# Performance work log

Hardware: AMD Instinct MI355X
Metric: run time of the kernel (lower is better)

## Reference

```python
import jax, jax.numpy as jnp
import numpy as np

B, L, C, K, S = 8, 4096, 512, 5, 8


def setup_inputs() -> dict:
    key = jax.random.key(0)
    ks = jax.random.split(key, 5)
    x = jax.random.normal(ks[0], (B, L, C), dtype=jnp.float32)
    # contiguous random partition of [0, L) into S segments per batch row
    rng = np.random.default_rng(0)
    cuts = np.sort(rng.integers(1, L, size=(B, S - 1)), axis=1)
    starts = np.concatenate([np.zeros((B, 1), np.int64), cuts.astype(np.int64)], axis=1)
    ends = np.concatenate([cuts.astype(np.int64), np.full((B, 1), L, np.int64)], axis=1)
    segment_boundaries = jnp.asarray(np.stack([starts, ends], axis=-1))  # [B,S,2]
    fan = 1.0 / np.sqrt(K)
    w_dw = jax.random.normal(ks[1], (C, K), dtype=jnp.float32) * fan
    b_dw = jax.random.normal(ks[2], (C,), dtype=jnp.float32) * 0.01
    w_pw = jax.random.normal(ks[3], (C, C), dtype=jnp.float32) * (1.0 / np.sqrt(C))
    b_pw = jax.random.normal(ks[4], (C,), dtype=jnp.float32) * 0.01
    return {"x": x, "segment_boundaries": segment_boundaries,
            "w_dw": w_dw, "b_dw": b_dw, "w_pw": w_pw, "b_pw": b_pw}


def reference(x, segment_boundaries, w_dw, b_dw, w_pw, b_pw):
    # x: [B,L,C]; segment_boundaries: [B,S,2]; w_dw: [C,K]; w_pw: [C_out,C_in]
    Bx, Lx, Cx = x.shape
    Kx = w_dw.shape[1]
    starts = segment_boundaries[..., 0]  # [B,S]
    ends = segment_boundaries[..., 1]    # [B,S]
    pos = jnp.arange(Lx)
    in_seg = (pos[None, None, :] >= starts[..., None]) & (pos[None, None, :] < ends[..., None])  # [B,S,L]
    covered = in_seg.any(axis=1)                                  # [B,L]
    seg_id = jnp.where(covered, jnp.argmax(in_seg, axis=1), -1)   # [B,L]

    # causal depthwise conv with left zero-pad per segment (no cross-segment leakage)
    acc = jnp.zeros_like(x)
    for d in range(Kx):  # d = how far back we look; tap index = K-1-d
        if d == 0:
            x_s, id_s = x, seg_id
        else:
            x_s = jnp.pad(x, ((0, 0), (d, 0), (0, 0)))[:, :Lx]
            id_s = jnp.pad(seg_id, ((0, 0), (d, 0)), constant_values=-2)[:, :Lx]
        m = ((seg_id == id_s) & covered).astype(x.dtype)          # [B,L]
        acc = acc + w_dw[:, Kx - 1 - d] * x_s * m[..., None]
    dw = acc + b_dw                                               # [B,L,C]
    pw = jnp.einsum('blc,dc->bld', dw, w_pw) + b_pw               # pointwise 1x1 conv
    return pw * covered[..., None].astype(x.dtype)                # zeros outside segments
```

## Files before the change

kernel.cpp:

```cpp
#include <hip/hip_runtime.h>
#include <hip/hip_bf16.h>

typedef __bf16 bf16;
typedef __bf16 bf16x2 __attribute__((ext_vector_type(2)));
typedef __bf16 bf16x4 __attribute__((ext_vector_type(4)));
typedef __bf16 bf16x8 __attribute__((ext_vector_type(8)));
typedef float f32x4 __attribute__((ext_vector_type(4)));

#define NB 8
#define L_ 4096
#define C_ 512
#define KW 5
#define NS 8
#define BM 128
#define BN 512
#define BK 32
#define NT 1024
#define KSTEPS 16

#define GLOAD_LDS16(g, l)                                                      \
  __builtin_amdgcn_global_load_lds(                                            \
      (const __attribute__((address_space(1))) void*)(g),                      \
      (__attribute__((address_space(3))) void*)(l), 16, 0, 0)

#define PRE_BARRIER(N)                                                         \
  do {                                                                         \
    asm volatile("s_waitcnt vmcnt(" #N ") lgkmcnt(0)" ::: "memory");           \
    __builtin_amdgcn_sched_barrier(0);                                         \
    __builtin_amdgcn_s_barrier();                                              \
    __builtin_amdgcn_sched_barrier(0);                                         \
  } while (0)

__global__ __launch_bounds__(256) void prep_kernel(
    const float* __restrict__ w_pw, const float* __restrict__ b_dw,
    const float* __restrict__ b_pw, bf16* __restrict__ wbf,
    float* __restrict__ bias2) {
  const int n = blockIdx.x;
  const int t = threadIdx.x;
  float2 v = *(const float2*)(w_pw + n * C_ + 2 * t);
  bf16x2 hv;
  hv[0] = (bf16)v.x;
  hv[1] = (bf16)v.y;
  *(bf16x2*)(wbf + n * C_ + 2 * t) = hv;
  float2 bb = *(const float2*)(b_dw + 2 * t);
  float s = v.x * bb.x + v.y * bb.y;
#pragma unroll
  for (int off = 32; off; off >>= 1) s += __shfl_down(s, off, 64);
  __shared__ float part[4];
  if ((t & 63) == 0) part[t >> 6] = s;
  __syncthreads();
  if (t == 0) bias2[n] = b_pw[n] + part[0] + part[1] + part[2] + part[3];
}

__global__ __launch_bounds__(NT) void fused_dwconv_gemm(
    const float* __restrict__ x, const int* __restrict__ segb,
    const float* __restrict__ w_dw, const bf16* __restrict__ wbf,
    const float* __restrict__ bias2, float* __restrict__ out) {
  __shared__ __align__(16) bf16 Bs[2][BN * BK];
  __shared__ __align__(16) bf16 dws[2][BM][40];
  __shared__ __align__(16) float xs[2][BM + 4][BK];
  __shared__ __align__(16) float wdt[KW][C_];
  __shared__ int segst[BM];

  const int t = threadIdx.x;
  const int lane = t & 63;
  const int wid = t >> 6;
  const int wm = wid >> 2;
  const int wn = wid & 3;

  const int b = blockIdx.x >> 5;
  const int l0 = (blockIdx.x & 31) << 7;

  if (t < C_) {
#pragma unroll
    for (int d = 0; d < KW; ++d) wdt[d][t] = w_dw[t * KW + d];
  }
  if (t < BM) {
    int l = l0 + t;
    const int* sb = segb + b * NS * 2;
    int st = 0;
#pragma unroll
    for (int s = 0; s < NS; ++s) {
      int a0 = sb[2 * s], a1 = sb[2 * s + 1];
      if (l >= a0 && l < a1) st = a0;
    }
    segst[t] = st;
  }
  __syncthreads();

  const int gr = t >> 3;
  const int gc = t & 7;
  int nv = (l0 + gr) - segst[gr];
  if (nv > 4) nv = 4;
  const bool fast = __all(nv == 4);

  const float* gxp = x + (size_t)(b * L_ + l0 + gr) * C_ + gc * 4;
  const int h = wid * 2 + lane;
  const int hr = h >> 3, hc = h & 7;
  int hl = l0 - 4 + hr;
  if (hl < 0) hl = 0;
  const float* gxh = x + (size_t)(b * L_ + hl) * C_ + hc * 4;

  const int nB0 = t >> 2, cB0 = t & 3;
  const int nB1 = (NT + t) >> 2, cB1 = t & 3;
  const bf16* gB0 = wbf + (size_t)nB0 * C_ + (cB0 ^ ((nB0 >> 1) & 3)) * 8;
  const bf16* gB1 = wbf + (size_t)nB1 * C_ + (cB1 ^ ((nB1 >> 1) & 3)) * 8;
  const int dB0 = (t & ~63) * 8;
  const int dB1 = (NT + (t & ~63)) * 8;

  f32x4 acc[2][8];
#pragma unroll
  for (int i = 0; i < 2; ++i)
#pragma unroll
    for (int j = 0; j < 8; ++j) acc[i][j] = (f32x4){0.f, 0.f, 0.f, 0.f};

  auto issueB = [&](int kk) {
    bf16* base = (bf16*)Bs[kk & 1];
    GLOAD_LDS16(gB0 + kk * BK, base + dB0);
    GLOAD_LDS16(gB1 + kk * BK, base + dB1);
  };

  auto issueGX = [&](int kk, float4& m4, float4& h4) {
    m4 = *(const float4*)(gxp + kk * BK);
    if (lane < 2) h4 = *(const float4*)(gxh + kk * BK);
  };

  auto stageX = [&](int kk, const float4& m4, const float4& h4) {
    const int p = kk & 1;
    *(float4*)&xs[p][gr + 4][gc * 4] = m4;
    if (lane < 2) *(float4*)&xs[p][hr][hc * 4] = h4;
  };

  auto conv = [&](int kk) {
    const int p = kk & 1;
    const int k0c = kk * BK + gc * 4;
    float w[KW][4];
#pragma unroll
    for (int m = 0; m < KW; ++m) {
      float4 wv = *(const float4*)&wdt[m][k0c];
      w[m][0] = wv.x; w[m][1] = wv.y; w[m][2] = wv.z; w[m][3] = wv.w;
    }
    if (!fast) {
#pragma unroll
      for (int m = 0; m < KW; ++m)
#pragma unroll
        for (int i = 0; i < 4; ++i)
          w[m][i] = (4 - m <= nv) ? w[m][i] : 0.f;
    }
    f32x4 a = (f32x4){0.f, 0.f, 0.f, 0.f};
#pragma unroll
    for (int m = 0; m < KW; ++m) {
      f32x4 xv = *(const f32x4*)&xs[p][gr + m][gc * 4];
#pragma unroll
      for (int i = 0; i < 4; ++i) a[i] = fmaf(w[m][i], xv[i], a[i]);
    }
    bf16x4 hq;
#pragma unroll
    for (int i = 0; i < 4; ++i) hq[i] = (bf16)a[i];
    *(bf16x4*)&dws[p][gr][gc * 4] = hq;
  };

  auto mma = [&](int kk) {
    const int p = kk & 1;
    bf16x8 afr[2];
#pragma unroll
    for (int mf = 0; mf < 2; ++mf)
      afr[mf] = *(const bf16x8*)&dws[p][wm * 32 + mf * 16 + (lane & 15)]
                                     [(lane >> 4) * 8];
#pragma unroll
    for (int nf = 0; nf < 8; ++nf) {
      const int nl = wn * 128 + nf * 16 + (lane & 15);
      const int ph = (lane >> 4) ^ ((nl >> 1) & 3);
      bf16x8 bfr = *(const bf16x8*)&Bs[p][nl * 32 + ph * 8];
#pragma unroll
      for (int mf = 0; mf < 2; ++mf)
        acc[mf][nf] = __builtin_amdgcn_mfma_f32_16x16x32_bf16(
            afr[mf], bfr, acc[mf][nf], 0, 0, 0);
    }
  };

  float4 gm0, gm1, gh0, gh1;

  issueGX(0, gm0, gh0);
  issueGX(1, gm1, gh1);
  stageX(0, gm0, gh0);
  issueGX(2, gm0, gh0);
  PRE_BARRIER(4);
  stageX(1, gm1, gh1);
  issueB(0);
  issueGX(3, gm1, gh1);
  conv(0);
  PRE_BARRIER(2);

#pragma unroll 1
  for (int k2 = 0; k2 < 12; k2 += 2) {
    issueB(k2 + 1);
    stageX(k2 + 2, gm0, gh0);
    issueGX(k2 + 4, gm0, gh0);
    conv(k2 + 1);
    mma(k2);
    PRE_BARRIER(2);

    issueB(k2 + 2);
    stageX(k2 + 3, gm1, gh1);
    issueGX(k2 + 5, gm1, gh1);
    conv(k2 + 2);
    mma(k2 + 1);
    PRE_BARRIER(2);
  }
  issueB(13);
  stageX(14, gm0, gh0);
  conv(13);
  mma(12);
  PRE_BARRIER(0);
  issueB(14);
  stageX(15, gm1, gh1);
  conv(14);
  mma(13);
  PRE_BARRIER(0);
  issueB(15);
  conv(15);
  mma(14);
  PRE_BARRIER(0);
  mma(15);

  const int col0 = wn * 128 + (lane & 15);
  float bia[8];
#pragma unroll
  for (int nf = 0; nf < 8; ++nf) bia[nf] = bias2[col0 + nf * 16];
  const int rb0 = l0 + wm * 32 + ((lane >> 4) << 2);
#pragma unroll
  for (int mf = 0; mf < 2; ++mf) {
#pragma unroll
    for (int i = 0; i < 4; ++i) {
      const int row = rb0 + mf * 16 + i;
      float* o = out + (size_t)(b * L_ + row) * C_ + col0;
#pragma unroll
      for (int nf = 0; nf < 8; ++nf) o[nf * 16] = acc[mf][nf][i] + bia[nf];
    }
  }
}

extern "C" void kernel_launch(void* const* d_in, const int* in_sizes, int n_in,
                              void* d_out, int out_size, void* d_ws,
                              size_t ws_size, hipStream_t stream) {
  const float* x = (const float*)d_in[0];
  const int* segb = (const int*)d_in[1];
  const float* w_dw = (const float*)d_in[2];
  const float* b_dw = (const float*)d_in[3];
  const float* w_pw = (const float*)d_in[4];
  const float* b_pw = (const float*)d_in[5];
  float* out = (float*)d_out;

  bf16* wbf = (bf16*)d_ws;
  float* bias2 = (float*)((char*)d_ws + C_ * C_ * 2);

  prep_kernel<<<C_, 256, 0, stream>>>(w_pw, b_dw, b_pw, wbf, bias2);
  fused_dwconv_gemm<<<NB * L_ / BM, NT, 0, stream>>>(x, segb, w_dw, wbf,
                                                     bias2, out);
}
```

Baseline: 46.59 us.

## Split fused depthwise conv and GEMM into separate conv and GEMM kernels

Adds a standalone conv kernel that computes the causal segmented depthwise conv with a sliding register window and writes a bf16 intermediate to workspace. A separate GEMM kernel then streams that intermediate and the bf16 weights into a triple-buffered LDS pipeline using direct global-to-LDS loads, with a different warp tiling. The aim is to take conv work and fp32 x staging out of the GEMM critical loop. The cost is an extra 32 MB bf16 round trip through global memory and one more launch. The old fused kernel remains as a fallback when the workspace is too small.

```diff
diff --git a/kernel.cpp b/kernel.cpp
--- a/kernel.cpp
+++ b/kernel.cpp
@@ -1,5 +1,6 @@
 #include <hip/hip_runtime.h>
 #include <hip/hip_bf16.h>
+#include <climits>
 
 typedef __bf16 bf16;
 typedef __bf16 bf16x2 __attribute__((ext_vector_type(2)));
@@ -12,16 +13,15 @@
 #define C_ 512
 #define KW 5
 #define NS 8
-#define BM 128
-#define BN 512
-#define BK 32
-#define NT 1024
-#define KSTEPS 16
 
 #define GLOAD_LDS16(g, l)                                                      \
   __builtin_amdgcn_global_load_lds(                                            \
       (const __attribute__((address_space(1))) void*)(g),                      \
       (__attribute__((address_space(3))) void*)(l), 16, 0, 0)
+#define GLOAD_LDS4(g, l)                                                       \
+  __builtin_amdgcn_global_load_lds(                                            \
+      (const __attribute__((address_space(1))) void*)(g),                      \
+      (__attribute__((address_space(3))) void*)(l), 4, 0, 0)
 
 #define PRE_BARRIER(N)                                                         \
   do {                                                                         \
@@ -52,6 +52,207 @@
   if (t == 0) bias2[n] = b_pw[n] + part[0] + part[1] + part[2] + part[3];
 }
 
+__global__ __launch_bounds__(256) void conv_kernel(
+    const float* __restrict__ x, const int* __restrict__ segb,
+    const float* __restrict__ w_dw, bf16* __restrict__ dwg) {
+  const int g = blockIdx.x * 256 + threadIdx.x;
+  const int quad = g & 127;
+  const int rest = g >> 7;
+  const int b = rest >> 7;
+  const int chunk = rest & 127;
+  const int l0 = chunk << 5;
+
+  float4 raw[5];
+#pragma unroll
+  for (int i = 0; i < 5; ++i)
+    raw[i] = *(const float4*)(w_dw + quad * 20 + i * 4);
+  f32x4 wt[5];
+#pragma unroll
+  for (int m = 0; m < 5; ++m)
+#pragma unroll
+    for (int i = 0; i < 4; ++i) {
+      const int f = i * 5 + m;
+      wt[m][i] = ((const float*)&raw[f >> 2])[f & 3];
+    }
+
+  const int* sb = segb + b * NS * 2;
+  int stv[NS];
+#pragma unroll
+  for (int s = 0; s < NS; ++s) stv[s] = sb[2 * s];
+  auto nxt = [&](int l) {
+    int nn = INT_MAX;
+#pragma unroll
+    for (int s = 0; s < NS; ++s)
+      nn = (stv[s] > l && stv[s] < nn) ? stv[s] : nn;
+    return nn;
+  };
+  int ns = nxt(l0 - 4);
+
+  const float* xbase = x + ((size_t)(b * L_ + l0)) * C_ + quad * 4;
+  bf16* dbase = dwg + ((size_t)(b * L_ + l0)) * C_ + quad * 4;
+
+  const f32x4 z4 = (f32x4){0.f, 0.f, 0.f, 0.f};
+  f32x4 w0 = z4, w1 = z4, w2 = z4, w3 = z4;
+
+#pragma unroll
+  for (int i = 0; i < 4; ++i) {
+    const int l = l0 - 4 + i;
+    f32x4 nv = z4;
+    if (l >= 0) nv = *(const f32x4*)(xbase + (ptrdiff_t)(i - 4) * C_);
+    if (l == ns) { w0 = z4; w1 = z4; w2 = z4; w3 = z4; ns = nxt(l); }
+    w0 = w1; w1 = w2; w2 = w3; w3 = nv;
+  }
+
+  auto dorow = [&](int l, f32x4& A, f32x4& B4, f32x4& Cc, f32x4& D,
+                   const f32x4& E, int off) {
+    if (l == ns) { A = z4; B4 = z4; Cc = z4; D = z4; ns = nxt(l); }
+    f32x4 r;
+#pragma unroll
+    for (int i = 0; i < 4; ++i) {
+      float a = A[i] * wt[0][i];
+      a = fmaf(B4[i], wt[1][i], a);
+      a = fmaf(Cc[i], wt[2][i], a);
+      a = fmaf(D[i], wt[3][i], a);
+      a = fmaf(E[i], wt[4][i], a);
+      r[i] = a;
+    }
+    bf16x4 h;
+#pragma unroll
+    for (int i = 0; i < 4; ++i) h[i] = (bf16)r[i];
+    *(bf16x4*)(dbase + (size_t)off * C_) = h;
+  };
+
+#pragma unroll 1
+  for (int g8 = 0; g8 < 8; ++g8) {
+    const int lb = l0 + g8 * 4;
+    f32x4 n0 = *(const f32x4*)(xbase + (ptrdiff_t)(g8 * 4 + 0) * C_);
+    f32x4 n1 = *(const f32x4*)(xbase + (ptrdiff_t)(g8 * 4 + 1) * C_);
+    f32x4 n2 = *(const f32x4*)(xbase + (ptrdiff_t)(g8 * 4 + 2) * C_);
+    f32x4 n3 = *(const f32x4*)(xbase + (ptrdiff_t)(g8 * 4 + 3) * C_);
+    dorow(lb + 0, w0, w1, w2, w3, n0, g8 * 4 + 0);
+    dorow(lb + 1, w1, w2, w3, n0, n1, g8 * 4 + 1);
+    dorow(lb + 2, w2, w3, n0, n1, n2, g8 * 4 + 2);
+    dorow(lb + 3, w3, n0, n1, n2, n3, g8 * 4 + 3);
+    w0 = n0; w1 = n1; w2 = n2; w3 = n3;
+  }
+}
+
+#define BMg 128
+#define BNg 512
+#define BKg 32
+__global__ __launch_bounds__(1024) void gemm_kernel(
+    const bf16* __restrict__ dwg, const bf16* __restrict__ wbf,
+    const float* __restrict__ bias2, float* __restrict__ out) {
+  __shared__ __align__(16) bf16 As[3][BMg * BKg];
+  __shared__ __align__(16) bf16 Bs[3][BNg * BKg];
+
+  const int t = threadIdx.x;
+  const int lane = t & 63;
+  const int wid = t >> 6;
+  const int wm = wid >> 3;
+  const int wn = wid & 7;
+
+  const int b = blockIdx.x >> 5;
+  const int l0 = (blockIdx.x & 31) << 7;
+
+  const int rA0 = t >> 4, wAi = t & 15;
+  const int rA1 = 64 + (t >> 4);
+  const size_t aoff0 = (size_t)(b * L_ + l0 + rA0) * C_ +
+                       ((((wAi >> 2) ^ ((rA0 >> 1) & 3)) << 3) + ((wAi & 3) << 1));
+  const size_t aoff1 = (size_t)(b * L_ + l0 + rA1) * C_ +
+                       ((((wAi >> 2) ^ ((rA1 >> 1) & 3)) << 3) + ((wAi & 3) << 1));
+  const int dA0 = wid * 128;
+  const int dA1 = 2048 + wid * 128;
+
+  const int nB0 = t >> 2, cB0 = t & 3;
+  const int nB1 = 256 + (t >> 2);
+  const bf16* gB0 = wbf + (size_t)nB0 * C_ + (cB0 ^ ((nB0 >> 1) & 3)) * 8;
+  const bf16* gB1 = wbf + (size_t)nB1 * C_ + (cB0 ^ ((nB1 >> 1) & 3)) * 8;
+  const int dB0 = (t & ~63) * 8;
+  const int dB1 = (1024 + (t & ~63)) * 8;
+
+  int aOff[4], bOff[4];
+#pragma unroll
+  for (int mf = 0; mf < 4; ++mf) {
+    const int row = wm * 64 + mf * 16 + (lane & 15);
+    aOff[mf] = row * 32 + (((lane >> 4) ^ ((row >> 1) & 3)) << 3);
+  }
+#pragma unroll
+  for (int nf = 0; nf < 4; ++nf) {
+    const int nl = wn * 64 + nf * 16 + (lane & 15);
+    bOff[nf] = nl * 32 + (((lane >> 4) ^ ((nl >> 1) & 3)) << 3);
+  }
+
+  f32x4 acc[4][4];
+#pragma unroll
+  for (int i = 0; i < 4; ++i)
+#pragma unroll
+    for (int j = 0; j < 4; ++j) acc[i][j] = (f32x4){0.f, 0.f, 0.f, 0.f};
+
+  auto issueAB = [&](int kk, int p) {
+    const int k0 = kk * BKg;
+    bf16* a = (bf16*)As[p];
+    bf16* bb = (bf16*)Bs[p];
+    GLOAD_LDS4(dwg + aoff0 + k0, a + dA0);
+    GLOAD_LDS4(dwg + aoff1 + k0, a + dA1);
+    GLOAD_LDS16(gB0 + k0, bb + dB0);
+    GLOAD_LDS16(gB1 + k0, bb + dB1);
+  };
+
+  auto mma = [&](int p) {
+    const bf16* a = (const bf16*)As[p];
+    const bf16* bb = (const bf16*)Bs[p];
+    bf16x8 afr[4];
+#pragma unroll
+    for (int mf = 0; mf < 4; ++mf) afr[mf] = *(const bf16x8*)(a + aOff[mf]);
+    __builtin_amdgcn_s_setprio(1);
+#pragma unroll
+    for (int nf = 0; nf < 4; ++nf) {
+      bf16x8 bfr = *(const bf16x8*)(bb + bOff[nf]);
+#pragma unroll
+      for (int mf = 0; mf < 4; ++mf)
+        acc[mf][nf] = __builtin_amdgcn_mfma_f32_16x16x32_bf16(
+            afr[mf], bfr, acc[mf][nf], 0, 0, 0);
+    }
+    __builtin_amdgcn_s_setprio(0);
+  };
+
+  issueAB(0, 0);
+  int pc = 0, pn = 1;
+#pragma unroll 1
+  for (int k = 0; k < 16; ++k) {
+    if (k < 15) {
+      issueAB(k + 1, pn);
+      PRE_BARRIER(4);
+    } else {
+      PRE_BARRIER(0);
+    }
+    mma(pc);
+    pc = (pc == 2) ? 0 : pc + 1;
+    pn = (pn == 2) ? 0 : pn + 1;
+  }
+
+  const int col0 = wn * 64 + (lane & 15);
+  float bia[4];
+#pragma unroll
+  for (int nf = 0; nf < 4; ++nf) bia[nf] = bias2[col0 + nf * 16];
+  const int rb0 = l0 + wm * 64 + ((lane >> 4) << 2);
+#pragma unroll
+  for (int mf = 0; mf < 4; ++mf) {
+#pragma unroll
+    for (int i = 0; i < 4; ++i) {
+      const int row = rb0 + mf * 16 + i;
+      float* o = out + (size_t)(b * L_ + row) * C_ + col0;
+#pragma unroll
+      for (int nf = 0; nf < 4; ++nf) o[nf * 16] = acc[mf][nf][i] + bia[nf];
+    }
+  }
+}
+
+#define BM 128
+#define BN 512
+#define BK 32
+#define NT 1024
 __global__ __launch_bounds__(NT) void fused_dwconv_gemm(
     const float* __restrict__ x, const int* __restrict__ segb,
     const float* __restrict__ w_dw, const bf16* __restrict__ wbf,
@@ -67,7 +268,6 @@
   const int wid = t >> 6;
   const int wm = wid >> 2;
   const int wn = wid & 3;
-
   const int b = blockIdx.x >> 5;
   const int l0 = (blockIdx.x & 31) << 7;
 
@@ -102,9 +302,9 @@
   const float* gxh = x + (size_t)(b * L_ + hl) * C_ + hc * 4;
 
   const int nB0 = t >> 2, cB0 = t & 3;
-  const int nB1 = (NT + t) >> 2, cB1 = t & 3;
+  const int nB1 = (NT + t) >> 2;
   const bf16* gB0 = wbf + (size_t)nB0 * C_ + (cB0 ^ ((nB0 >> 1) & 3)) * 8;
-  const bf16* gB1 = wbf + (size_t)nB1 * C_ + (cB1 ^ ((nB1 >> 1) & 3)) * 8;
+  const bf16* gB1 = wbf + (size_t)nB1 * C_ + (cB0 ^ ((nB1 >> 1) & 3)) * 8;
   const int dB0 = (t & ~63) * 8;
   const int dB1 = (NT + (t & ~63)) * 8;
 
@@ -119,18 +319,15 @@
     GLOAD_LDS16(gB0 + kk * BK, base + dB0);
     GLOAD_LDS16(gB1 + kk * BK, base + dB1);
   };
-
   auto issueGX = [&](int kk, float4& m4, float4& h4) {
     m4 = *(const float4*)(gxp + kk * BK);
     if (lane < 2) h4 = *(const float4*)(gxh + kk * BK);
   };
-
   auto stageX = [&](int kk, const float4& m4, const float4& h4) {
     const int p = kk & 1;
     *(float4*)&xs[p][gr + 4][gc * 4] = m4;
     if (lane < 2) *(float4*)&xs[p][hr][hc * 4] = h4;
   };
-
   auto conv = [&](int kk) {
     const int p = kk & 1;
     const int k0c = kk * BK + gc * 4;
@@ -144,8 +341,7 @@
 #pragma unroll
       for (int m = 0; m < KW; ++m)
 #pragma unroll
-        for (int i = 0; i < 4; ++i)
-          w[m][i] = (4 - m <= nv) ? w[m][i] : 0.f;
+        for (int i = 0; i < 4; ++i) w[m][i] = (4 - m <= nv) ? w[m][i] : 0.f;
     }
     f32x4 a = (f32x4){0.f, 0.f, 0.f, 0.f};
 #pragma unroll
@@ -159,7 +355,6 @@
     for (int i = 0; i < 4; ++i) hq[i] = (bf16)a[i];
     *(bf16x4*)&dws[p][gr][gc * 4] = hq;
   };
-
   auto mma = [&](int kk) {
     const int p = kk & 1;
     bf16x8 afr[2];
@@ -180,7 +375,6 @@
   };
 
   float4 gm0, gm1, gh0, gh1;
-
   issueGX(0, gm0, gh0);
   issueGX(1, gm1, gh1);
   stageX(0, gm0, gh0);
@@ -191,7 +385,6 @@
   issueGX(3, gm1, gh1);
   conv(0);
   PRE_BARRIER(2);
-
 #pragma unroll 1
   for (int k2 = 0; k2 < 12; k2 += 2) {
     issueB(k2 + 1);
@@ -200,7 +393,6 @@
     conv(k2 + 1);
     mma(k2);
     PRE_BARRIER(2);
-
     issueB(k2 + 2);
     stageX(k2 + 3, gm1, gh1);
     issueGX(k2 + 5, gm1, gh1);
@@ -254,8 +446,17 @@
 
   bf16* wbf = (bf16*)d_ws;
   float* bias2 = (float*)((char*)d_ws + C_ * C_ * 2);
+  bf16* dwg = (bf16*)((char*)d_ws + (1 << 20));
+
+  const size_t need = (size_t)(1 << 20) + (size_t)NB * L_ * C_ * 2;
 
   prep_kernel<<<C_, 256, 0, stream>>>(w_pw, b_dw, b_pw, wbf, bias2);
-  fused_dwconv_gemm<<<NB * L_ / BM, NT, 0, stream>>>(x, segb, w_dw, wbf,
-                                                     bias2, out);
+  if (ws_size >= need) {
+    conv_kernel<<<(NB * 128 * (L_ / 32)) / 256, 256, 0, stream>>>(x, segb,
+                                                                  w_dw, dwg);
+    gemm_kernel<<<NB * L_ / BMg, 1024, 0, stream>>>(dwg, wbf, bias2, out);
+  } else {
+    fused_dwconv_gemm<<<NB * L_ / BM, NT, 0, stream>>>(x, segb, w_dw, wbf,
+                                                       bias2, out);
+  }
 }
```

Result: slower. 53.53 us (+14.9%).
